# Kernel tuning notes

Measured on AMD Instinct MI355X. Metric: run time of the kernel, lower is better.

## Reference

```python
import jax, jax.numpy as jnp
import numpy as np

N_LAYERS = 20
EPS = 1e-7      # GENConv eps added to relu'd messages
BN_EPS = 1e-5   # torch BatchNorm1d default eps
N_NODES, N_EDGES, N_GRAPHS, D, H = 100_000, 400_000, 4096, 128, 256


def _bn(x, g, b):
    # BatchNorm1d in training mode: batch statistics over the node dim
    mu = jnp.mean(x, axis=0)
    var = jnp.var(x, axis=0)
    return (x - mu) * jax.lax.rsqrt(var + BN_EPS) * g + b


def setup_inputs() -> dict:
    key = jax.random.key(0)
    ks = jax.random.split(key, 12)
    L = N_LAYERS
    rn = lambda k, s, sc: jax.random.normal(k, s, dtype=jnp.float32) * sc
    return dict(
        x=jax.random.randint(ks[0], (N_NODES, 9), 0, 2, dtype=jnp.int32),
        edge_index=jax.random.randint(ks[1], (2, N_EDGES), 0, N_NODES, dtype=jnp.int32),
        edge_attr=jax.random.randint(ks[2], (N_EDGES, 3), 0, 2, dtype=jnp.int32),
        batch=jnp.sort(jax.random.randint(ks[3], (N_NODES,), 0, N_GRAPHS, dtype=jnp.int32)),
        # AtomEncoder: 9 tables (max size 119), padded into one array
        atom_emb=rn(ks[4], (9, 119, D), 0.1),
        # per-layer BondEncoder: 3 tables (sizes 5,6,2) padded to 6
        bond_emb=rn(ks[5], (L, 3, 6, D), 0.1),
        W1=rn(ks[6], (L, D, H), 0.05), b1=jnp.zeros((L, H), jnp.float32),
        g1=jnp.ones((L, H), jnp.float32), be1=jnp.zeros((L, H), jnp.float32),
        W2=rn(ks[7], (L, H, H), 0.05), b2=jnp.zeros((L, H), jnp.float32),
        g2=jnp.ones((L, H), jnp.float32), be2=jnp.zeros((L, H), jnp.float32),
        W3=rn(ks[8], (L, H, D), 0.05), b3=jnp.zeros((L, D), jnp.float32),
        t=jnp.ones((L,), jnp.float32),
        norm_g=jnp.ones((L, D), jnp.float32), norm_b=jnp.zeros((L, D), jnp.float32),
        predW=rn(ks[9], (D, 1), 0.05), predb=jnp.zeros((1,), jnp.float32),
    )


def _gen_conv(h, src, dst, edge_attr, bond_l, W1, b1, g1, be1, W2, b2, g2, be2, W3, b3, t):
    N = h.shape[0]
    # BondEncoder: sum of 3 embedding lookups
    eemb = bond_l[0][edge_attr[:, 0]] + bond_l[1][edge_attr[:, 1]] + bond_l[2][edge_attr[:, 2]]
    msg = jax.nn.relu(h[src] + eemb) + EPS            # [E, D]
    # scatter_softmax over destination nodes, per channel, temperature t
    scaled = msg * t
    mx = jax.ops.segment_max(scaled, dst, num_segments=N)
    mx = jnp.where(jnp.isfinite(mx), mx, 0.0)         # isolated nodes -> -inf guard
    ex = jnp.exp(scaled - mx[dst])
    denom = jax.ops.segment_sum(ex, dst, num_segments=N)
    w = ex / jnp.maximum(denom[dst], EPS)
    m = jax.ops.segment_sum(msg * w, dst, num_segments=N)
    hh = h + m
    # MLP channels [D, 2D, 2D, D], batch norm + relu on hidden layers, last linear
    a = jax.nn.relu(_bn(hh @ W1 + b1, g1, be1))
    a = jax.nn.relu(_bn(a @ W2 + b2, g2, be2))
    return a @ W3 + b3


def reference(x, edge_index, edge_attr, batch, atom_emb, bond_emb, W1, b1, g1, be1,
              W2, b2, g2, be2, W3, b3, t, norm_g, norm_b, predW, predb):
    N = x.shape[0]
    src, dst = edge_index[0], edge_index[1]
    # AtomEncoder: sum of 9 embedding lookups
    h = atom_emb[0][x[:, 0]]
    for i in range(1, 9):
        h = h + atom_emb[i][x[:, i]]
    lp = lambda l: (bond_emb[l], W1[l], b1[l], g1[l], be1[l], W2[l], b2[l],
                    g2[l], be2[l], W3[l], b3[l], t[l])
    # res+ block (dropout omitted: eval mode)
    h = _gen_conv(h, src, dst, edge_attr, *lp(0))
    for l in range(1, N_LAYERS):
        h2 = jax.nn.relu(_bn(h, norm_g[l - 1], norm_b[l - 1]))
        h = _gen_conv(h2, src, dst, edge_attr, *lp(l)) + h
    h = _bn(h, norm_g[N_LAYERS - 1], norm_b[N_LAYERS - 1])
    # global mean pool over graphs
    cnt = jax.ops.segment_sum(jnp.ones((N, 1), jnp.float32), batch, num_segments=N_GRAPHS)
    hg = jax.ops.segment_sum(h, batch, num_segments=N_GRAPHS) / jnp.maximum(cnt, 1.0)
    return hg @ predW + predb                          # [N_GRAPHS, 1]
```

## Files before the change

### kernel.cpp

```cpp
#include <hip/hip_runtime.h>
#include <math.h>

#define GEPS 1e-7f
#define BNEPS 1e-5f
#define NCOPY 32
#define CSTR 1536

typedef unsigned short u16;
typedef unsigned int   u32;

typedef _Float16 f16x8 __attribute__((ext_vector_type(8)));
typedef float    f32x4 __attribute__((ext_vector_type(4)));

__device__ __forceinline__ float h2f(u16 u){
  _Float16 x = __builtin_bit_cast(_Float16, u); return (float)x;
}
__device__ __forceinline__ u16 f2h(float f){
  _Float16 x = (_Float16)f; return __builtin_bit_cast(u16, x);
}

typedef __attribute__((address_space(1))) const void* as1p;
typedef __attribute__((address_space(3))) void*       as3p;
__device__ __forceinline__ void dma16(const u16* g, _Float16* l){
  __builtin_amdgcn_global_load_lds((as1p)g, (as3p)l, 16, 0, 0);
}

__global__ __launch_bounds__(256) void k_zero_i(int* __restrict__ p, int n){
  int i = blockIdx.x*256 + threadIdx.x;
  if (i < n) p[i] = 0;
}
__global__ __launch_bounds__(256) void k_zero_f(float* __restrict__ p, int n){
  int i = blockIdx.x*256 + threadIdx.x;
  if (i < n) p[i] = 0.f;
}

__global__ __launch_bounds__(256) void k_hist(const int* __restrict__ dst, int E,
                                              int* __restrict__ cnt){
  int e = blockIdx.x*256 + threadIdx.x;
  if (e < E) atomicAdd(&cnt[dst[e]], 1);
}

__global__ __launch_bounds__(256) void k_blocksum(const int* __restrict__ cnt, int N,
                                                  int* __restrict__ part){
  __shared__ int s[256];
  int t = threadIdx.x, i = blockIdx.x*256 + t;
  s[t] = (i < N) ? cnt[i] : 0;
  __syncthreads();
  for (int off = 128; off > 0; off >>= 1){
    if (t < off) s[t] += s[t + off];
    __syncthreads();
  }
  if (t == 0) part[blockIdx.x] = s[0];
}

__global__ __launch_bounds__(1024) void k_scanpart(int* __restrict__ part, int NB){
  __shared__ int s[1024];
  int t = threadIdx.x;
  int v = (t < NB) ? part[t] : 0;
  s[t] = v;
  __syncthreads();
  for (int off = 1; off < 1024; off <<= 1){
    int u = (t >= off) ? s[t-off] : 0;
    __syncthreads();
    s[t] += u;
    __syncthreads();
  }
  if (t < NB) part[t] = s[t] - v;
}

__global__ __launch_bounds__(256) void k_scanapply(const int* __restrict__ cnt,
    const int* __restrict__ part, int N, int E,
    int* __restrict__ offs, int* __restrict__ cursor){
  __shared__ int s[256];
  int t = threadIdx.x, i = blockIdx.x*256 + t;
  int v = (i < N) ? cnt[i] : 0;
  s[t] = v;
  __syncthreads();
  for (int off = 1; off < 256; off <<= 1){
    int u = (t >= off) ? s[t-off] : 0;
    __syncthreads();
    s[t] += u;
    __syncthreads();
  }
  int ex = part[blockIdx.x] + s[t] - v;
  if (i < N){
    offs[i]   = ex;
    cursor[i] = ex;
    if (i == N-1) offs[N] = ex + v;
  }
}

__global__ __launch_bounds__(256) void k_scatter(const int* __restrict__ src,
    const int* __restrict__ dst, const int* __restrict__ attr, int E,
    int* __restrict__ cursor, int* __restrict__ esort){
  int e = blockIdx.x*256 + threadIdx.x;
  if (e >= E) return;
  int d = dst[e];
  int pos = atomicAdd(&cursor[d], 1);
  int comb = attr[3*(size_t)e]*12 + attr[3*(size_t)e+1]*2 + attr[3*(size_t)e+2];
  esort[pos] = (src[e] & 0x1ffff) | (comb << 17);
}

__global__ __launch_bounds__(256) void k_comb(const float* __restrict__ bond_emb,
    float* __restrict__ comb, int total){
  int id = blockIdx.x*256 + threadIdx.x;
  if (id >= total) return;
  int d = id & 127;
  int c = (id >> 7) % 72;
  int l = (id >> 7) / 72;
  int a0 = c/12, a1 = (c/2)%6, a2 = c&1;
  const float* b = bond_emb + (size_t)l*3*6*128;
  comb[id] = b[a0*128 + d] + b[(6 + a1)*128 + d] + b[(12 + a2)*128 + d];
}

__global__ __launch_bounds__(256) void k_wtrans(const float* __restrict__ W,
    u16* __restrict__ Wt, int K, int Nout, int total){
  int id = blockIdx.x*256 + threadIdx.x;
  if (id >= total) return;
  int k   = id % K;
  int rem = id / K;
  int n   = rem % Nout;
  int l   = rem / Nout;
  Wt[id] = f2h(W[((size_t)l*K + k)*Nout + n]);
}

__global__ __launch_bounds__(256) void k_atom(const int* __restrict__ x,
    const float* __restrict__ emb, float* __restrict__ h, u16* __restrict__ h16, int N){
  int d = threadIdx.x & 127;
  int n = (blockIdx.x << 1) + (threadIdx.x >> 7);
  if (n >= N) return;
  float s = 0.f;
  #pragma unroll
  for (int i = 0; i < 9; ++i){
    int idx = x[(size_t)n*9 + i];
    s += emb[((size_t)i*119 + idx)*128 + d];
  }
  h[(size_t)n*128 + d]   = s;
  h16[(size_t)n*128 + d] = f2h(s);
}

__global__ __launch_bounds__(256) void k_redstats(const float* __restrict__ Cl,
                                                  float* __restrict__ out){
  int t = threadIdx.x;
  float s = 0.f;
  #pragma unroll
  for (int c = 0; c < NCOPY; ++c) s += Cl[c*CSTR + 1024 + t];
  out[t] = s;
}

template<bool PRE_BN>
__global__ __launch_bounds__(256)
void k_edge(const u16* __restrict__ h16,
    const int* __restrict__ offs, const int* __restrict__ esort,
    const float* __restrict__ comb,
    const float* __restrict__ tptr,
    const float* __restrict__ ssum_, const float* __restrict__ ssq_,
    const float* __restrict__ g, const float* __restrict__ b,
    u16* __restrict__ hh, int N, float invN){
  __shared__ float sg[128], sv[128];
  int tid = threadIdx.x;
  if (PRE_BN){
    if (tid < 128){
      float mu  = ssum_[tid]*invN;
      float var = fmaxf(ssq_[tid]*invN - mu*mu, 0.f);
      float rs  = rsqrtf(var + BNEPS);
      float s   = g[tid]*rs;
      sg[tid] = s;
      sv[tid] = b[tid] - mu*s;
    }
    __syncthreads();
  }
  int lane = tid & 63;
  int n = (blockIdx.x << 2) + (tid >> 6);
  if (n >= N) return;
  int c0 = lane << 1;
  float tl = *tptr;
  float sg0=1.f, sv0=0.f, sg1=1.f, sv1=0.f;
  if (PRE_BN){ sg0=sg[c0]; sv0=sv[c0]; sg1=sg[c0+1]; sv1=sv[c0+1]; }

  int s0 = offs[n], s1 = offs[n+1];
  float den0 = 0.f, acc0 = 0.f, den1 = 0.f, acc1 = 0.f;
  if (s0 < s1){
    int se = esort[s0];
    u32 hv = *(const u32*)(h16 + (size_t)(se & 0x1ffff)*128 + c0);
    float2 ev = *(const float2*)(comb + (se >> 17)*128 + c0);
    for (int e = s0; e < s1; ++e){
      u32 hvN = hv; float2 evN = ev;
      if (e + 1 < s1){
        int seN = esort[e+1];
        hvN = *(const u32*)(h16 + (size_t)(seN & 0x1ffff)*128 + c0);
        evN = *(const float2*)(comb + (seN >> 17)*128 + c0);
      }
      float x0 = h2f((u16)(hv & 0xffff));
      float x1 = h2f((u16)(hv >> 16));
      if (PRE_BN){
        x0 = fmaxf(x0*sg0 + sv0, 0.f);
        x1 = fmaxf(x1*sg1 + sv1, 0.f);
      }
      float m0 = fmaxf(x0 + ev.x, 0.f) + GEPS;
      float m1 = fmaxf(x1 + ev.y, 0.f) + GEPS;
      float p0 = __expf(m0*tl);
      float p1 = __expf(m1*tl);
      den0 += p0; acc0 += p0*m0;
      den1 += p1; acc1 += p1*m1;
      hv = hvN; ev = evN;
    }
  }
  u32 hv = *(const u32*)(h16 + (size_t)n*128 + c0);
  float x0 = h2f((u16)(hv & 0xffff));
  float x1 = h2f((u16)(hv >> 16));
  if (PRE_BN){
    x0 = fmaxf(x0*sg0 + sv0, 0.f);
    x1 = fmaxf(x1*sg1 + sv1, 0.f);
  }
  float r0 = x0 + acc0 / fmaxf(den0, GEPS);
  float r1 = x1 + acc1 / fmaxf(den1, GEPS);
  u32 pk = (u32)f2h(r0) | ((u32)f2h(r1) << 16);
  *((u32*)hh + (size_t)n*64 + lane) = pk;
}

template<bool TRANSFORM, bool OUT32>
__global__ __launch_bounds__(256)
void k_gemm(const u16* __restrict__ A, int lda,
            const u16* __restrict__ Wt,
            const float* __restrict__ bias,
            const float* __restrict__ sIn, const float* __restrict__ qIn,
            const float* __restrict__ gam, const float* __restrict__ bet,
            const float* __restrict__ resid,
            void* __restrict__ outv, int ldo,
            u16* __restrict__ out16,
            float* __restrict__ sOut, float* __restrict__ qOut,
            int M, int K){
  __shared__ __align__(16) _Float16 As[2][2048];
  __shared__ __align__(16) _Float16 Bs[2][4096];
  __shared__ float sc[256], shv[256];

  int tid = threadIdx.x;
  int lane = tid & 63;
  int wn   = tid >> 6;
  int quad = lane >> 4, ln = lane & 15;
  int mBase = blockIdx.x * 64;
  int cBase = blockIdx.y * 128;

  int fA = tid >> 6, lA = tid & 63;
  int kA = (lA >> 4) << 3;
  int rA = mBase + fA*16 + (lA & 15); if (rA >= M) rA = M - 1;
  const u16* apA = A + (size_t)rA*lda + kA;
  int dc0 = tid, dc1 = 256 + tid;
  int f0 = dc0 >> 6, l20 = dc0 & 63;
  int f1 = dc1 >> 6, l21 = dc1 & 63;
  int kB0 = (l20 >> 4) << 3, kB1 = (l21 >> 4) << 3;
  const u16* bp0 = Wt + (size_t)(cBase + f0*16 + (l20 & 15))*K + kB0;
  const u16* bp1 = Wt + (size_t)(cBase + f1*16 + (l21 & 15))*K + kB1;

  dma16(apA, &As[0][dc0*8]);
  dma16(bp0, &Bs[0][dc0*8]);
  dma16(bp1, &Bs[0][dc1*8]);

  if (TRANSFORM){
    float inv = 1.f/(float)M;
    for (int k = tid; k < K; k += 256){
      float s_ = 0.f, q_ = 0.f;
      #pragma unroll
      for (int c = 0; c < NCOPY; ++c){ s_ += sIn[c*CSTR + k]; q_ += qIn[c*CSTR + k]; }
      float mu  = s_*inv;
      float var = fmaxf(q_*inv - mu*mu, 0.f);
      float rs  = rsqrtf(var + BNEPS);
      float sg  = gam[k]*rs;
      sc[k]  = sg;
      shv[k] = bet[k] - mu*sg;
    }
  }

  f32x4 acc[4][2];
  #pragma unroll
  for (int i = 0; i < 4; ++i)
    #pragma unroll
    for (int j = 0; j < 2; ++j)
      acc[i][j] = (f32x4){0.f,0.f,0.f,0.f};

  int kTiles = K >> 5;
  for (int kt = 0; kt < kTiles; ++kt){
    __syncthreads();
    int cb = kt & 1, nbuf = cb ^ 1;
    if (kt + 1 < kTiles){
      int k1 = (kt + 1) << 5;
      dma16(apA + k1, &As[nbuf][dc0*8]);
      dma16(bp0 + k1, &Bs[nbuf][dc0*8]);
      dma16(bp1 + k1, &Bs[nbuf][dc1*8]);
    }
    f16x8 af[4], bf[2];
    #pragma unroll
    for (int i = 0; i < 4; ++i)
      af[i] = *(const f16x8*)(&As[cb][i*512 + lane*8]);
    if (TRANSFORM){
      int kb = kt*32 + quad*8;
      f32x4 s0 = *(const f32x4*)(&sc[kb]);
      f32x4 s1 = *(const f32x4*)(&sc[kb+4]);
      f32x4 v0 = *(const f32x4*)(&shv[kb]);
      f32x4 v1 = *(const f32x4*)(&shv[kb+4]);
      #pragma unroll
      for (int i = 0; i < 4; ++i){
        f16x8 a = af[i], o;
        o[0] = (_Float16)fmaxf((float)a[0]*s0[0] + v0[0], 0.f);
        o[1] = (_Float16)fmaxf((float)a[1]*s0[1] + v0[1], 0.f);
        o[2] = (_Float16)fmaxf((float)a[2]*s0[2] + v0[2], 0.f);
        o[3] = (_Float16)fmaxf((float)a[3]*s0[3] + v0[3], 0.f);
        o[4] = (_Float16)fmaxf((float)a[4]*s1[0] + v1[0], 0.f);
        o[5] = (_Float16)fmaxf((float)a[5]*s1[1] + v1[1], 0.f);
        o[6] = (_Float16)fmaxf((float)a[6]*s1[2] + v1[2], 0.f);
        o[7] = (_Float16)fmaxf((float)a[7]*s1[3] + v1[3], 0.f);
        af[i] = o;
      }
    }
    #pragma unroll
    for (int j = 0; j < 2; ++j)
      bf[j] = *(const f16x8*)(&Bs[cb][(2*wn + j)*512 + lane*8]);
    #pragma unroll
    for (int i = 0; i < 4; ++i)
      #pragma unroll
      for (int j = 0; j < 2; ++j)
        acc[i][j] = __builtin_amdgcn_mfma_f32_16x16x32_f16(af[i], bf[j], acc[i][j], 0, 0, 0);
  }

  float bv[2];
  #pragma unroll
  for (int j = 0; j < 2; ++j) bv[j] = bias[cBase + (2*wn + j)*16 + ln];
  float ps[2] = {0,0}, pq[2] = {0,0};

  #pragma unroll
  for (int i = 0; i < 4; ++i){
    #pragma unroll
    for (int r = 0; r < 4; ++r){
      int row = mBase + 16*i + quad*4 + r;
      if (row < M){
        size_t base = (size_t)row*ldo;
        #pragma unroll
        for (int j = 0; j < 2; ++j){
          int col = cBase + (2*wn + j)*16 + ln;
          float v = acc[i][j][r] + bv[j];
          if (OUT32){
            float* out = (float*)outv;
            if (resid) v += resid[base + col];
            out[base + col] = v;
            if (out16) out16[base + col] = f2h(v);
            ps[j] += v; pq[j] += v*v;
          } else {
            u16* out = (u16*)outv;
            u16 q = f2h(v);
            out[base + col] = q;
            float vr = h2f(q);
            ps[j] += vr; pq[j] += vr*vr;
          }
        }
      }
    }
  }
  #pragma unroll
  for (int j = 0; j < 2; ++j){
    float s = ps[j], q = pq[j];
    s += __shfl_xor(s, 16, 64);  q += __shfl_xor(q, 16, 64);
    s += __shfl_xor(s, 32, 64);  q += __shfl_xor(q, 32, 64);
    if (quad == 0){
      int cof = (blockIdx.x & (NCOPY-1))*CSTR + cBase + (2*wn + j)*16 + ln;
      atomicAdd(&sOut[cof], s);
      atomicAdd(&qOut[cof], q);
    }
  }
}

__global__ __launch_bounds__(256) void k_pool(const float* __restrict__ h,
    const float* __restrict__ ssum, const float* __restrict__ ssq,
    const float* __restrict__ g, const float* __restrict__ b,
    const float* __restrict__ predW, const int* __restrict__ batch,
    float* __restrict__ pool, float* __restrict__ cnt, int N){
  int lane = threadIdx.x & 63;
  int n = (blockIdx.x << 2) + (threadIdx.x >> 6);
  if (n >= N) return;
  float inv = 1.f / (float)N;
  float v = 0.f;
  #pragma unroll
  for (int d = lane; d < 128; d += 64){
    float mu  = ssum[d]*inv;
    float var = fmaxf(ssq[d]*inv - mu*mu, 0.f);
    float rs  = rsqrtf(var + BNEPS);
    float bn  = (h[(size_t)n*128 + d] - mu)*(g[d]*rs) + b[d];
    v += bn * predW[d];
  }
  #pragma unroll
  for (int off = 32; off > 0; off >>= 1) v += __shfl_down(v, off, 64);
  if (lane == 0){
    int gi = batch[n];
    atomicAdd(&pool[gi], v);
    atomicAdd(&cnt[gi], 1.f);
  }
}

__global__ __launch_bounds__(256) void k_final(const float* __restrict__ pool,
    const float* __restrict__ cnt, const float* __restrict__ predb,
    float* __restrict__ out, int G){
  int g = blockIdx.x*256 + threadIdx.x;
  if (g < G) out[g] = pool[g] / fmaxf(cnt[g], 1.f) + predb[0];
}

extern "C" void kernel_launch(void* const* d_in, const int* in_sizes, int n_in,
                              void* d_out, int out_size, void* d_ws, size_t ws_size,
                              hipStream_t stream){
  const int*   x        = (const int*)d_in[0];
  const int*   eidx     = (const int*)d_in[1];
  const int*   eattr    = (const int*)d_in[2];
  const int*   batch    = (const int*)d_in[3];
  const float* atom_emb = (const float*)d_in[4];
  const float* bond_emb = (const float*)d_in[5];
  const float* W1 = (const float*)d_in[6];
  const float* b1 = (const float*)d_in[7];
  const float* g1 = (const float*)d_in[8];
  const float* be1= (const float*)d_in[9];
  const float* W2 = (const float*)d_in[10];
  const float* b2 = (const float*)d_in[11];
  const float* g2 = (const float*)d_in[12];
  const float* be2= (const float*)d_in[13];
  const float* W3 = (const float*)d_in[14];
  const float* b3 = (const float*)d_in[15];
  const float* tt = (const float*)d_in[16];
  const float* ng = (const float*)d_in[17];
  const float* nb = (const float*)d_in[18];
  const float* predW = (const float*)d_in[19];
  const float* predb = (const float*)d_in[20];
  float* out = (float*)d_out;

  const int N = in_sizes[3];
  const int E = in_sizes[1] / 2;
  const int L = in_sizes[16];
  const int G = out_size;
  const int D = 128, H = 256;
  const float invN = 1.f / (float)N;

  char* ws = (char*)d_ws;
  size_t off = 0;
  auto carve = [&](size_t bytes)->void*{
    void* p = ws + off;
    off += (bytes + 511) & ~(size_t)511;
    return p;
  };
  float* h   = (float*)carve((size_t)N*D*4);
  u16*   y1  = (u16*)  carve((size_t)N*H*2);
  u16*   y2  = (u16*)  carve((size_t)N*H*2);
  u16*   hh  = y2;
  u16*   h16 = y1;
  u16*   Wt1 = (u16*) carve((size_t)L*H*D*2);
  u16*   Wt2 = (u16*) carve((size_t)L*H*H*2);
  u16*   Wt3 = (u16*) carve((size_t)L*D*H*2);
  int*  offs   = (int*)carve((size_t)(N+1)*4);
  int*  cursor = (int*)carve((size_t)N*4);
  int*  cnt    = (int*)carve((size_t)N*4);
  int*  part   = (int*)carve(1024*4);
  int*  esort  = (int*)carve((size_t)E*4);
  float* comb  = (float*)carve((size_t)L*72*128*4);
  float* stats = (float*)carve((size_t)L*NCOPY*CSTR*4);
  float* fstat = (float*)carve((size_t)L*256*4);
  float* pool = (float*)carve((size_t)G*4);
  float* cntg = (float*)carve((size_t)G*4);

  int NB = (N + 255) / 256;

  k_zero_i   <<<NB, 256, 0, stream>>>(cnt, N);
  k_hist     <<<(E+255)/256, 256, 0, stream>>>(eidx + E, E, cnt);
  k_blocksum <<<NB, 256, 0, stream>>>(cnt, N, part);
  k_scanpart <<<1, 1024, 0, stream>>>(part, NB);
  k_scanapply<<<NB, 256, 0, stream>>>(cnt, part, N, E, offs, cursor);
  k_scatter  <<<(E+255)/256, 256, 0, stream>>>(eidx, eidx + E, eattr, E, cursor, esort);
  k_atom     <<<(N+1)/2, 256, 0, stream>>>(x, atom_emb, h, h16, N);
  k_zero_f   <<<(L*NCOPY*CSTR+255)/256, 256, 0, stream>>>(stats, L*NCOPY*CSTR);
  k_comb     <<<((L*72*128)+255)/256, 256, 0, stream>>>(bond_emb, comb, L*72*128);

  k_wtrans<<<((L*H*D)+255)/256, 256, 0, stream>>>(W1, Wt1, D, H, L*H*D);
  k_wtrans<<<((L*H*H)+255)/256, 256, 0, stream>>>(W2, Wt2, H, H, L*H*H);
  k_wtrans<<<((L*D*H)+255)/256, 256, 0, stream>>>(W3, Wt3, H, D, L*D*H);

  int mb = (N + 63) / 64;
  int eb = (N + 3) / 4;
  for (int l = 0; l < L; ++l){
    float* Cl = stats + (size_t)l*NCOPY*CSTR;
    const float* combl = comb + (size_t)l*72*128;
    if (l == 0){
      k_edge<false><<<eb, 256, 0, stream>>>(h16, offs, esort, combl, tt + l,
          nullptr, nullptr, nullptr, nullptr, hh, N, invN);
    } else {
      float* fs = fstat + (size_t)(l-1)*256;
      k_edge<true><<<eb, 256, 0, stream>>>(h16, offs, esort, combl, tt + l,
          fs, fs + 128, ng + (size_t)(l-1)*D, nb + (size_t)(l-1)*D,
          hh, N, invN);
    }
    k_gemm<false,false><<<dim3(mb,2), 256, 0, stream>>>(hh, D,
        Wt1 + (size_t)l*H*D, b1 + (size_t)l*H,
        nullptr, nullptr, nullptr, nullptr, nullptr,
        y1, H, nullptr, Cl + 0, Cl + 256, N, D);
    k_gemm<true,false><<<dim3(mb,2), 256, 0, stream>>>(y1, H,
        Wt2 + (size_t)l*H*H, b2 + (size_t)l*H,
        Cl + 0, Cl + 256, g1 + (size_t)l*H, be1 + (size_t)l*H, nullptr,
        y2, H, nullptr, Cl + 512, Cl + 768, N, H);
    k_gemm<true,true><<<dim3(mb,1), 256, 0, stream>>>(y2, H,
        Wt3 + (size_t)l*D*H, b3 + (size_t)l*D,
        Cl + 512, Cl + 768, g2 + (size_t)l*H, be2 + (size_t)l*H,
        (l ? h : nullptr),
        h, D, h16, Cl + 1024, Cl + 1152, N, H);
    k_redstats<<<1, 256, 0, stream>>>(Cl, fstat + (size_t)l*256);
  }

  float* fsL = fstat + (size_t)(L-1)*256;
  k_zero_f<<<(G+255)/256, 256, 0, stream>>>(pool, G);
  k_zero_f<<<(G+255)/256, 256, 0, stream>>>(cntg, G);
  k_pool  <<<(N+3)/4, 256, 0, stream>>>(h, fsL, fsL + 128,
      ng + (size_t)(L-1)*D, nb + (size_t)(L-1)*D, predW, batch, pool, cntg, N);
  k_final <<<(G+255)/256, 256, 0, stream>>>(pool, cntg, predb, out, G);
}
```

Measured before the change: 4.958 ms.

## Enlarge GEMM block tile to 256 rows and reduce BN stats in LDS

The GEMM block tile grows from 64x128 to 256x128. Each wave now computes 64 rows by all 128 columns instead of 64 rows by 32 columns, so each B-tile load is reused across more rows and fewer blocks refetch the weights. The per-wave column statistics are first summed in shared memory (reusing the A buffer) and then written with one atomic per column per block, which cuts atomic traffic. In exchange the block uses more registers (32 accumulators per thread) and more LDS, which may lower occupancy, and with 256-row tiles there are fewer blocks to spread across the CUs.

```diff
diff --git a/kernel.cpp b/kernel.cpp
--- a/kernel.cpp
+++ b/kernel.cpp
@@ -231,31 +231,43 @@
             u16* __restrict__ out16,
             float* __restrict__ sOut, float* __restrict__ qOut,
             int M, int K){
-  __shared__ __align__(16) _Float16 As[2][2048];
+  __shared__ __align__(16) _Float16 As[2][8192];
   __shared__ __align__(16) _Float16 Bs[2][4096];
   __shared__ float sc[256], shv[256];
+  float* redS = (float*)(&As[0][0]);
+  float* redQ = redS + 512;
 
   int tid = threadIdx.x;
   int lane = tid & 63;
-  int wn   = tid >> 6;
+  int w    = tid >> 6;
   int quad = lane >> 4, ln = lane & 15;
-  int mBase = blockIdx.x * 64;
+  int mBase = blockIdx.x * 256;
   int cBase = blockIdx.y * 128;
 
-  int fA = tid >> 6, lA = tid & 63;
-  int kA = (lA >> 4) << 3;
-  int rA = mBase + fA*16 + (lA & 15); if (rA >= M) rA = M - 1;
-  const u16* apA = A + (size_t)rA*lda + kA;
-  int dc0 = tid, dc1 = 256 + tid;
-  int f0 = dc0 >> 6, l20 = dc0 & 63;
-  int f1 = dc1 >> 6, l21 = dc1 & 63;
-  int kB0 = (l20 >> 4) << 3, kB1 = (l21 >> 4) << 3;
-  const u16* bp0 = Wt + (size_t)(cBase + f0*16 + (l20 & 15))*K + kB0;
-  const u16* bp1 = Wt + (size_t)(cBase + f1*16 + (l21 & 15))*K + kB1;
-
-  dma16(apA, &As[0][dc0*8]);
-  dma16(bp0, &Bs[0][dc0*8]);
-  dma16(bp1, &Bs[0][dc1*8]);
+  const u16* apA[4]; int dcA[4];
+  #pragma unroll
+  for (int s = 0; s < 4; ++s){
+    int dc = s*256 + tid;
+    dcA[s] = dc;
+    int f = dc >> 6, l2 = dc & 63;
+    int kk = (l2 >> 4) << 3;
+    int r = mBase + f*16 + (l2 & 15); if (r >= M) r = M - 1;
+    apA[s] = A + (size_t)r*lda + kk;
+  }
+  const u16* bpB[2]; int dcB[2];
+  #pragma unroll
+  for (int s = 0; s < 2; ++s){
+    int dc = s*256 + tid;
+    dcB[s] = dc;
+    int f = dc >> 6, l2 = dc & 63;
+    int kk = (l2 >> 4) << 3;
+    bpB[s] = Wt + (size_t)(cBase + f*16 + (l2 & 15))*K + kk;
+  }
+
+  #pragma unroll
+  for (int s = 0; s < 4; ++s) dma16(apA[s], &As[0][dcA[s]*8]);
+  #pragma unroll
+  for (int s = 0; s < 2; ++s) dma16(bpB[s], &Bs[0][dcB[s]*8]);
 
   if (TRANSFORM){
     float inv = 1.f/(float)M;
@@ -272,11 +284,11 @@
     }
   }
 
-  f32x4 acc[4][2];
+  f32x4 acc[4][8];
   #pragma unroll
   for (int i = 0; i < 4; ++i)
     #pragma unroll
-    for (int j = 0; j < 2; ++j)
+    for (int j = 0; j < 8; ++j)
       acc[i][j] = (f32x4){0.f,0.f,0.f,0.f};
 
   int kTiles = K >> 5;
@@ -285,14 +297,15 @@
     int cb = kt & 1, nbuf = cb ^ 1;
     if (kt + 1 < kTiles){
       int k1 = (kt + 1) << 5;
-      dma16(apA + k1, &As[nbuf][dc0*8]);
-      dma16(bp0 + k1, &Bs[nbuf][dc0*8]);
-      dma16(bp1 + k1, &Bs[nbuf][dc1*8]);
-    }
-    f16x8 af[4], bf[2];
+      #pragma unroll
+      for (int s = 0; s < 4; ++s) dma16(apA[s] + k1, &As[nbuf][dcA[s]*8]);
+      #pragma unroll
+      for (int s = 0; s < 2; ++s) dma16(bpB[s] + k1, &Bs[nbuf][dcB[s]*8]);
+    }
+    f16x8 af[4];
     #pragma unroll
     for (int i = 0; i < 4; ++i)
-      af[i] = *(const f16x8*)(&As[cb][i*512 + lane*8]);
+      af[i] = *(const f16x8*)(&As[cb][(4*w + i)*512 + lane*8]);
     if (TRANSFORM){
       int kb = kt*32 + quad*8;
       f32x4 s0 = *(const f32x4*)(&sc[kb]);
@@ -314,30 +327,31 @@
       }
     }
     #pragma unroll
-    for (int j = 0; j < 2; ++j)
-      bf[j] = *(const f16x8*)(&Bs[cb][(2*wn + j)*512 + lane*8]);
-    #pragma unroll
-    for (int i = 0; i < 4; ++i)
+    for (int j = 0; j < 8; ++j){
+      f16x8 bf = *(const f16x8*)(&Bs[cb][j*512 + lane*8]);
       #pragma unroll
-      for (int j = 0; j < 2; ++j)
-        acc[i][j] = __builtin_amdgcn_mfma_f32_16x16x32_f16(af[i], bf[j], acc[i][j], 0, 0, 0);
-  }
-
-  float bv[2];
-  #pragma unroll
-  for (int j = 0; j < 2; ++j) bv[j] = bias[cBase + (2*wn + j)*16 + ln];
-  float ps[2] = {0,0}, pq[2] = {0,0};
+      for (int i = 0; i < 4; ++i)
+        acc[i][j] = __builtin_amdgcn_mfma_f32_16x16x32_f16(af[i], bf, acc[i][j], 0, 0, 0);
+    }
+  }
+
+  float bv[8];
+  #pragma unroll
+  for (int j = 0; j < 8; ++j) bv[j] = bias[cBase + j*16 + ln];
+  float ps[8], pq[8];
+  #pragma unroll
+  for (int j = 0; j < 8; ++j){ ps[j] = 0.f; pq[j] = 0.f; }
 
   #pragma unroll
   for (int i = 0; i < 4; ++i){
     #pragma unroll
     for (int r = 0; r < 4; ++r){
-      int row = mBase + 16*i + quad*4 + r;
+      int row = mBase + 64*w + 16*i + quad*4 + r;
       if (row < M){
         size_t base = (size_t)row*ldo;
         #pragma unroll
-        for (int j = 0; j < 2; ++j){
-          int col = cBase + (2*wn + j)*16 + ln;
+        for (int j = 0; j < 8; ++j){
+          int col = cBase + j*16 + ln;
           float v = acc[i][j][r] + bv[j];
           if (OUT32){
             float* out = (float*)outv;
@@ -357,15 +371,23 @@
     }
   }
   #pragma unroll
-  for (int j = 0; j < 2; ++j){
+  for (int j = 0; j < 8; ++j){
     float s = ps[j], q = pq[j];
     s += __shfl_xor(s, 16, 64);  q += __shfl_xor(q, 16, 64);
     s += __shfl_xor(s, 32, 64);  q += __shfl_xor(q, 32, 64);
     if (quad == 0){
-      int cof = (blockIdx.x & (NCOPY-1))*CSTR + cBase + (2*wn + j)*16 + ln;
-      atomicAdd(&sOut[cof], s);
-      atomicAdd(&qOut[cof], q);
-    }
+      int col = j*16 + ln;
+      redS[w*128 + col] = s;
+      redQ[w*128 + col] = q;
+    }
+  }
+  __syncthreads();
+  if (tid < 128){
+    float s = redS[tid] + redS[128 + tid] + redS[256 + tid] + redS[384 + tid];
+    float q = redQ[tid] + redQ[128 + tid] + redQ[256 + tid] + redQ[384 + tid];
+    int cof = (blockIdx.x & (NCOPY-1))*CSTR + cBase + tid;
+    atomicAdd(&sOut[cof], s);
+    atomicAdd(&qOut[cof], q);
   }
 }
 
@@ -478,7 +500,7 @@
   k_wtrans<<<((L*H*H)+255)/256, 256, 0, stream>>>(W2, Wt2, H, H, L*H*H);
   k_wtrans<<<((L*D*H)+255)/256, 256, 0, stream>>>(W3, Wt3, H, D, L*D*H);
 
-  int mb = (N + 63) / 64;
+  int mb = (N + 255) / 256;
   int eb = (N + 3) / 4;
   for (int l = 0; l < L; ++l){
     float* Cl = stats + (size_t)l*NCOPY*CSTR;
```

New measurement: 5.821 ms. 1.17x slower.
